# Kernel optimization log

Measured on AMD Instinct MI355X. Metric: run time of the kernel, lower is better.

Reference implementation:

```python
import jax, jax.numpy as jnp
import numpy as np

N = 100000   # neuron_count (nodes)
D = 128      # node feature dim
E = 2000000  # edges
NW = 8       # number of distinct weight matrices


def setup_inputs() -> dict:
    key = jax.random.key(0)
    k1, k2, k3, k4, k5 = jax.random.split(key, 5)
    x = jax.random.normal(k1, (N, D), dtype=jnp.float32)
    W = jax.random.normal(k2, (NW, D, D), dtype=jnp.float32) * 0.02
    u = jax.random.randint(k3, (E,), 0, N)      # edge source nodes
    v = jax.random.randint(k4, (E,), 0, N)      # edge dest nodes
    widx = jax.random.randint(k5, (E,), 0, NW)  # per-edge weight index
    return {"x": x, "W": W, "u": u, "v": v, "widx": widx}


def reference(x, W, u, v, widx):
    # DGL update_all: per-edge message m_e = W[widx_e] @ x[u_e], then
    # x_out[v] = tanh(sum of incoming m). Because the message is linear in
    # x_src, we aggregate source features per (weight-index, dest-node)
    # segment first, then apply each weight matrix once (grouped GEMM):
    #   out[v, i] = tanh( sum_w sum_j W[w, i, j] * S[w, v, j] )
    seg = widx * N + v                                   # combined segment id
    S = jax.ops.segment_sum(x[u], seg, num_segments=NW * N)  # [NW*N, D]
    S = S.reshape(NW, N, D)
    out = jnp.einsum("wij,wvj->vi", W, S)                # [N, D]
    # zero in-degree nodes: DGL gives 0 feature; tanh(0)=0, consistent.
    return jnp.tanh(out)
```

## Files before the change

### kernel.cpp

```cpp
#include <hip/hip_runtime.h>
#include <math.h>

#define D 128

typedef __attribute__((ext_vector_type(8))) short bf8;
typedef __attribute__((ext_vector_type(4))) float f32x4;

__device__ __forceinline__ unsigned short f2bf_rne(float f) {
  unsigned u = __float_as_uint(f);
  unsigned r = (u + 0x7FFFu + ((u >> 16) & 1u)) >> 16;
  return (unsigned short)r;
}
__device__ __forceinline__ float bf2f(unsigned short h) {
  return __uint_as_float(((unsigned)h) << 16);
}
__device__ __forceinline__ float bflo(unsigned p) {
  return __uint_as_float(p << 16);
}
__device__ __forceinline__ float bfhi(unsigned p) {
  return __uint_as_float(p & 0xFFFF0000u);
}

__global__ __launch_bounds__(256) void prep_kernel(
    const float* __restrict__ x, unsigned short* __restrict__ xbf,
    long long xTotal, int xcGrid,
    const int* __restrict__ v, const int* __restrict__ widx,
    int* __restrict__ cnt2, int* __restrict__ rank,
    long long E, long long N) {
  if (blockIdx.x < (unsigned)xcGrid) {
    long long i0 = ((long long)blockIdx.x * 256 + threadIdx.x) * 8;
    if (i0 + 8 > xTotal) return;
    float4 f0 = *(const float4*)(x + i0);
    float4 f1 = *(const float4*)(x + i0 + 4);
    unsigned short o[8];
    o[0] = f2bf_rne(f0.x); o[1] = f2bf_rne(f0.y);
    o[2] = f2bf_rne(f0.z); o[3] = f2bf_rne(f0.w);
    o[4] = f2bf_rne(f1.x); o[5] = f2bf_rne(f1.y);
    o[6] = f2bf_rne(f1.z); o[7] = f2bf_rne(f1.w);
    *(bf8*)(xbf + i0) = *(bf8*)o;
  } else {
    long long base = (long long)(blockIdx.x - xcGrid) * 1024;
    #pragma unroll
    for (int k = 0; k < 4; ++k) {
      long long e = base + k * 256 + threadIdx.x;
      if (e < E) {
        long long seg = (long long)widx[e] * N + v[e];
        rank[e] = atomicAdd(&cnt2[seg], 1);
      }
    }
  }
}

__global__ __launch_bounds__(1024) void scanA_kernel(
    const int* __restrict__ cnt2, int* __restrict__ starts2,
    int* __restrict__ blkSums, long long NB2) {
  __shared__ int part[1024];
  int tid = threadIdx.x;
  long long base = (long long)blockIdx.x * 4096 + tid * 4;
  int c[4];
  #pragma unroll
  for (int i = 0; i < 4; ++i)
    c[i] = (base + i < NB2) ? cnt2[base + i] : 0;
  int loc[4];
  int sum = 0;
  #pragma unroll
  for (int i = 0; i < 4; ++i) { loc[i] = sum; sum += c[i]; }
  part[tid] = sum;
  __syncthreads();
  for (int off = 1; off < 1024; off <<= 1) {
    int val = (tid >= off) ? part[tid - off] : 0;
    __syncthreads();
    part[tid] += val;
    __syncthreads();
  }
  int excl = (tid == 0) ? 0 : part[tid - 1];
  #pragma unroll
  for (int i = 0; i < 4; ++i)
    if (base + i < NB2) starts2[base + i] = excl + loc[i];
  if (tid == 1023) blkSums[blockIdx.x] = part[1023];
}

__global__ __launch_bounds__(1024) void scanC_kernel(
    int* __restrict__ starts2, const int* __restrict__ blkSums,
    long long NB2, int Etot, int nBlk) {
  __shared__ int part[256];
  int tid = threadIdx.x;
  if (tid < 256) part[tid] = (tid < nBlk) ? blkSums[tid] : 0;
  __syncthreads();
  for (int off = 1; off < 256; off <<= 1) {
    int val = 0;
    if (tid < 256 && tid >= off) val = part[tid - off];
    __syncthreads();
    if (tid < 256) part[tid] += val;
    __syncthreads();
  }
  int off = (blockIdx.x == 0) ? 0 : part[blockIdx.x - 1];
  long long base = (long long)blockIdx.x * 4096 + tid * 4;
  #pragma unroll
  for (int i = 0; i < 4; ++i) {
    long long idx = base + i;
    if (idx < NB2) starts2[idx] += off;
  }
  if (blockIdx.x == 0 && tid == 0) starts2[NB2] = Etot;
}

__global__ __launch_bounds__(256) void scatwc_kernel(
    const float* __restrict__ W, unsigned short* __restrict__ Wp, int NW,
    int wpGrid,
    const int* __restrict__ u, const int* __restrict__ v,
    const int* __restrict__ widx, const int* __restrict__ rank,
    const int* __restrict__ starts2, int* __restrict__ sortedU,
    long long E, long long N) {
  if (blockIdx.x < (unsigned)wpGrid) {
    int idx = blockIdx.x * 256 + threadIdx.x;
    if (idx >= NW * 2048) return;
    int lane = idx & 63;
    int ks = (idx >> 6) & 3;
    int n  = (idx >> 8) & 7;
    int w  = idx >> 11;
    int row = n * 16 + (lane & 15);
    int col = ks * 32 + (lane >> 4) * 8;
    const float* src = W + (size_t)w * D * D + (size_t)row * D + col;
    unsigned short hi[8], re[8];
    #pragma unroll
    for (int e = 0; e < 8; ++e) {
      float f = src[e];
      unsigned short h = f2bf_rne(f);
      hi[e] = h;
      re[e] = f2bf_rne(f - bf2f(h));
    }
    int frag = (w * 8 + n) * 4 + ks;
    unsigned short* dst = Wp + (size_t)frag * 1024 + lane * 8;
    *(bf8*)dst = *(bf8*)hi;
    *(bf8*)(dst + 512) = *(bf8*)re;
  } else {
    long long base = (long long)(blockIdx.x - wpGrid) * 1024;
    #pragma unroll
    for (int k = 0; k < 4; ++k) {
      long long e = base + k * 256 + threadIdx.x;
      if (e < E) {
        long long seg = (long long)widx[e] * N + v[e];
        int pos = starts2[seg] + rank[e];
        sortedU[pos] = u[e] * 32;
      }
    }
  }
}

__global__ __launch_bounds__(256) void gather_pack_kernel(
    const unsigned short* __restrict__ xbf, const int* __restrict__ starts2,
    const int* __restrict__ sortedU, unsigned short* __restrict__ Sp,
    long long N, long long nt16) {
  __shared__ float T[16][132];
  int tid = threadIdx.x;
  long long w = blockIdx.y;
  long long rt = blockIdx.x;
  long long r0 = rt * 16;
  int grp = tid >> 5;
  int lane = tid & 31;

  #pragma unroll
  for (int rr = 0; rr < 2; ++rr) {
    int rloc = grp + rr * 8;
    long long r = r0 + rloc;
    float ax = 0.f, ay = 0.f, az = 0.f, aw = 0.f;
    if (r < N) {
      long long seg = w * N + r;
      int s0 = starts2[seg];
      int s1 = starts2[seg + 1];
      const uint2* xb = (const uint2*)xbf;
      for (int i = s0; i < s1; i += 4) {
        int uu[4];
        uint2 av[4];
        #pragma unroll
        for (int k = 0; k < 4; ++k)
          if (i + k < s1) uu[k] = sortedU[i + k];
        #pragma unroll
        for (int k = 0; k < 4; ++k)
          if (i + k < s1) av[k] = xb[(size_t)uu[k] + lane];
        #pragma unroll
        for (int k = 0; k < 4; ++k) {
          if (i + k < s1) {
            ax += bflo(av[k].x); ay += bfhi(av[k].x);
            az += bflo(av[k].y); aw += bfhi(av[k].y);
          }
        }
      }
    }
    *(float4*)&T[rloc][lane * 4] = make_float4(ax, ay, az, aw);
  }
  __syncthreads();

  int ks = tid >> 6;
  int l = tid & 63;
  const float* src = &T[l & 15][ks * 32 + (l >> 4) * 8];
  unsigned short o[8];
  #pragma unroll
  for (int e = 0; e < 8; ++e) o[e] = f2bf_rne(src[e]);
  size_t frag = ((size_t)w * nt16 + rt) * 4 + ks;
  *(bf8*)(Sp + frag * 512 + (size_t)l * 8) = *(bf8*)o;
}

template<int NWT>
__global__ __launch_bounds__(256, 3) void mfma_gemm_kernel(
    const unsigned short* __restrict__ Sp, const unsigned short* __restrict__ Wp,
    float* __restrict__ out, long long N, long long nt16, int NWdyn) {
  int tid = threadIdx.x;
  int wv = tid >> 6;
  int wr = wv >> 1;
  int wc = wv & 1;
  int l = tid & 63;
  long long rtBase = (long long)blockIdx.x * 4 + wr * 2;

  const unsigned short* SA = Sp + (size_t)rtBase * 2048 + (size_t)l * 8;
  const unsigned short* WB = Wp + (size_t)wc * 16384 + (size_t)l * 8;
  const size_t wStrideS = (size_t)nt16 * 2048;

  f32x4 acc[2][4];
  #pragma unroll
  for (int m = 0; m < 2; ++m)
    #pragma unroll
    for (int n = 0; n < 4; ++n) acc[m][n] = (f32x4)(0.f);

  if (NWT == 8) {
    bf8 a[4][2], bh[2][4], br[2][4];
    {
      a[0][0] = *(const bf8*)(SA);
      a[0][1] = *(const bf8*)(SA + 2048);
      a[1][0] = *(const bf8*)(SA + 512);
      a[1][1] = *(const bf8*)(SA + 512 + 2048);
      a[2][0] = *(const bf8*)(SA + 1024);
      a[2][1] = *(const bf8*)(SA + 1024 + 2048);
      #pragma unroll
      for (int n = 0; n < 4; ++n) {
        bh[0][n] = *(const bf8*)(WB + n * 4096);
        br[0][n] = *(const bf8*)(WB + n * 4096 + 512);
      }
    }
    #pragma unroll
    for (int s = 0; s < 32; ++s) {
      const int abuf = s & 3;
      const int bbuf = s & 1;
      if (s + 3 < 32) {
        const int t = s + 3, w2 = t >> 2, ks2 = t & 3;
        const unsigned short* sa = SA + (size_t)w2 * wStrideS + ks2 * 512;
        a[(s + 3) & 3][0] = *(const bf8*)(sa);
        a[(s + 3) & 3][1] = *(const bf8*)(sa + 2048);
      }
      if (s + 1 < 32) {
        const int t = s + 1, w2 = t >> 2, ks2 = t & 3;
        const unsigned short* wb = WB + (size_t)w2 * 32768 + ks2 * 1024;
        #pragma unroll
        for (int n = 0; n < 4; ++n) {
          bh[bbuf ^ 1][n] = *(const bf8*)(wb + n * 4096);
          br[bbuf ^ 1][n] = *(const bf8*)(wb + n * 4096 + 512);
        }
      }
      #pragma unroll
      for (int n = 0; n < 4; ++n)
        #pragma unroll
        for (int m = 0; m < 2; ++m) {
          acc[m][n] = __builtin_amdgcn_mfma_f32_16x16x32_bf16(a[abuf][m], bh[bbuf][n], acc[m][n], 0, 0, 0);
          acc[m][n] = __builtin_amdgcn_mfma_f32_16x16x32_bf16(a[abuf][m], br[bbuf][n], acc[m][n], 0, 0, 0);
        }
    }
  } else {
    for (int w = 0; w < NWdyn; ++w) {
      #pragma unroll
      for (int ks = 0; ks < 4; ++ks) {
        const unsigned short* sa = SA + (size_t)w * wStrideS + ks * 512;
        bf8 a0 = *(const bf8*)(sa);
        bf8 a1 = *(const bf8*)(sa + 2048);
        const unsigned short* wb = WB + (size_t)w * 32768 + ks * 1024;
        #pragma unroll
        for (int n = 0; n < 4; ++n) {
          bf8 bh0 = *(const bf8*)(wb + n * 4096);
          bf8 br0 = *(const bf8*)(wb + n * 4096 + 512);
          acc[0][n] = __builtin_amdgcn_mfma_f32_16x16x32_bf16(a0, bh0, acc[0][n], 0, 0, 0);
          acc[1][n] = __builtin_amdgcn_mfma_f32_16x16x32_bf16(a1, bh0, acc[1][n], 0, 0, 0);
          acc[0][n] = __builtin_amdgcn_mfma_f32_16x16x32_bf16(a0, br0, acc[0][n], 0, 0, 0);
          acc[1][n] = __builtin_amdgcn_mfma_f32_16x16x32_bf16(a1, br0, acc[1][n], 0, 0, 0);
        }
      }
    }
  }

  int lrow = l & 15;
  int crow0 = (l >> 4) * 4;
  #pragma unroll
  for (int m = 0; m < 2; ++m) {
    long long vbase = (rtBase + m) * 16 + crow0;
    #pragma unroll
    for (int rr = 0; rr < 4; ++rr) {
      long long v = vbase + rr;
      if (v < N) {
        float* op = out + v * D + wc * 64 + lrow;
        #pragma unroll
        for (int n = 0; n < 4; ++n) op[n * 16] = tanhf(acc[m][n][rr]);
      }
    }
  }
}

extern "C" void kernel_launch(void* const* d_in, const int* in_sizes, int n_in,
                              void* d_out, int out_size, void* d_ws, size_t ws_size,
                              hipStream_t stream) {
  const float* x    = (const float*)d_in[0];
  const float* W    = (const float*)d_in[1];
  const int*   u    = (const int*)d_in[2];
  const int*   v    = (const int*)d_in[3];
  const int*   widx = (const int*)d_in[4];

  long long N  = (long long)in_sizes[0] / D;
  int       NW = in_sizes[1] / (D * D);
  long long E  = (long long)in_sizes[2];
  float* out = (float*)d_out;

  long long NB2 = (long long)NW * N;
  int gemmBlocks = (int)((N + 63) / 64);
  long long NpadA = (long long)gemmBlocks * 64;
  long long nt16 = NpadA / 16;
  int nScanBlk = (int)((NB2 + 4095) / 4096);
  long long xTotal = N * D;

  char* ws = (char*)d_ws;
  int* cnt2    = (int*)ws;                        ws += (size_t)NB2 * sizeof(int);
  int* starts2 = (int*)ws;                        ws += ((size_t)NB2 + 1) * sizeof(int);
  int* rank    = (int*)ws;                        ws += (size_t)E * sizeof(int);
  int* blkSums = (int*)ws;                        ws += 256 * sizeof(int);
  int* sortedU = (int*)ws;                        ws += (size_t)E * sizeof(int);
  ws = (char*)(((uintptr_t)ws + 255) & ~(uintptr_t)255);
  unsigned short* Wp = (unsigned short*)ws;       ws += (size_t)NW * 32768 * 2;
  ws = (char*)(((uintptr_t)ws + 255) & ~(uintptr_t)255);
  unsigned short* xbf = (unsigned short*)ws;      ws += (size_t)xTotal * 2;
  ws = (char*)(((uintptr_t)ws + 255) & ~(uintptr_t)255);
  unsigned short* Sp = (unsigned short*)ws;       ws += (size_t)NW * NpadA * D * 2;
  (void)ws_size;

  dim3 blk(256);
  int edgeGrid4 = (int)((E + 1023) / 1024);
  int wpGrid = (NW * 2048 + 255) / 256;
  int xcGrid = (int)((xTotal / 8 + 255) / 256);

  hipMemsetAsync(cnt2, 0, (size_t)NB2 * sizeof(int), stream);
  prep_kernel<<<xcGrid + edgeGrid4, blk, 0, stream>>>(
      x, xbf, xTotal, xcGrid, v, widx, cnt2, rank, E, N);
  scanA_kernel<<<nScanBlk, 1024, 0, stream>>>(cnt2, starts2, blkSums, NB2);
  scanC_kernel<<<nScanBlk, 1024, 0, stream>>>(starts2, blkSums, NB2,
                                              (int)E, nScanBlk);
  scatwc_kernel<<<wpGrid + edgeGrid4, blk, 0, stream>>>(
      W, Wp, NW, wpGrid, u, v, widx, rank, starts2, sortedU, E, N);
  dim3 ggrid((unsigned)nt16, (unsigned)NW);
  gather_pack_kernel<<<ggrid, blk, 0, stream>>>(xbf, starts2, sortedU, Sp, N, nt16);
  if (NW == 8) {
    mfma_gemm_kernel<8><<<gemmBlocks, blk, 0, stream>>>(
        Sp, Wp, out, N, nt16, NW);
  } else {
    mfma_gemm_kernel<0><<<gemmBlocks, blk, 0, stream>>>(
        Sp, Wp, out, N, nt16, NW);
  }
}
```

Before: 397.4 us.

## Stage GEMM A-tiles into LDS via async global_load_lds double buffering

The grouped GEMM kernel now copies each weight slice's S tile straight into shared memory with global_load_lds, double-buffered across the eight weight indices with a block barrier per stage, instead of having every wave load its A fragments into registers. This is meant to cut register pressure and overlap the A-tile fetch with MFMA work, and the occupancy hint rises from 3 to 4 blocks per CU. The cost is 32 KB of LDS per block and a __syncthreads every weight step. The per-lane A register prefetch is replaced by LDS reads.

```diff
diff --git a/kernel.cpp b/kernel.cpp
--- a/kernel.cpp
+++ b/kernel.cpp
@@ -5,6 +5,8 @@
 
 typedef __attribute__((ext_vector_type(8))) short bf8;
 typedef __attribute__((ext_vector_type(4))) float f32x4;
+typedef const __attribute__((address_space(1))) unsigned short* gas_us;
+typedef __attribute__((address_space(3))) unsigned short* las_us;
 
 __device__ __forceinline__ unsigned short f2bf_rne(float f) {
   unsigned u = __float_as_uint(f);
@@ -202,17 +204,17 @@
 }
 
 template<int NWT>
-__global__ __launch_bounds__(256, 3) void mfma_gemm_kernel(
+__global__ __launch_bounds__(256, 4) void mfma_gemm_kernel(
     const unsigned short* __restrict__ Sp, const unsigned short* __restrict__ Wp,
     float* __restrict__ out, long long N, long long nt16, int NWdyn) {
+  __shared__ unsigned short Al[2][8192];
   int tid = threadIdx.x;
   int wv = tid >> 6;
   int wr = wv >> 1;
   int wc = wv & 1;
   int l = tid & 63;
-  long long rtBase = (long long)blockIdx.x * 4 + wr * 2;
-
-  const unsigned short* SA = Sp + (size_t)rtBase * 2048 + (size_t)l * 8;
+  long long rtBlk = (long long)blockIdx.x * 4;
+
   const unsigned short* WB = Wp + (size_t)wc * 16384 + (size_t)l * 8;
   const size_t wStrideS = (size_t)nt16 * 2048;
 
@@ -223,48 +225,62 @@
     for (int n = 0; n < 4; ++n) acc[m][n] = (f32x4)(0.f);
 
   if (NWT == 8) {
-    bf8 a[4][2], bh[2][4], br[2][4];
-    {
-      a[0][0] = *(const bf8*)(SA);
-      a[0][1] = *(const bf8*)(SA + 2048);
-      a[1][0] = *(const bf8*)(SA + 512);
-      a[1][1] = *(const bf8*)(SA + 512 + 2048);
-      a[2][0] = *(const bf8*)(SA + 1024);
-      a[2][1] = *(const bf8*)(SA + 1024 + 2048);
+    #define STAGE_A(W_, B_)                                                  \
+      {                                                                      \
+        const unsigned short* g =                                            \
+            Sp + ((size_t)(W_) * nt16 + rtBlk) * 2048;                       \
+        _Pragma("unroll")                                                    \
+        for (int c = 0; c < 4; ++c) {                                        \
+          int chunk = wv * 4 + c;                                            \
+          __builtin_amdgcn_global_load_lds(                                  \
+              (gas_us)(g + chunk * 512 + l * 8),                             \
+              (las_us)&Al[B_][chunk * 512], 16, 0, 0);                       \
+        }                                                                    \
+      }
+
+    STAGE_A(0, 0)
+    __syncthreads();
+
+    bf8 bh[2][4], br[2][4];
+    #pragma unroll
+    for (int n = 0; n < 4; ++n) {
+      bh[0][n] = *(const bf8*)(WB + n * 4096);
+      br[0][n] = *(const bf8*)(WB + n * 4096 + 512);
+    }
+
+    #pragma unroll
+    for (int w = 0; w < 8; ++w) {
+      if (w < 7) STAGE_A(w + 1, (w + 1) & 1)
+      const int b = w & 1;
+      int rtl = wr * 2;
       #pragma unroll
-      for (int n = 0; n < 4; ++n) {
-        bh[0][n] = *(const bf8*)(WB + n * 4096);
-        br[0][n] = *(const bf8*)(WB + n * 4096 + 512);
-      }
-    }
-    #pragma unroll
-    for (int s = 0; s < 32; ++s) {
-      const int abuf = s & 3;
-      const int bbuf = s & 1;
-      if (s + 3 < 32) {
-        const int t = s + 3, w2 = t >> 2, ks2 = t & 3;
-        const unsigned short* sa = SA + (size_t)w2 * wStrideS + ks2 * 512;
-        a[(s + 3) & 3][0] = *(const bf8*)(sa);
-        a[(s + 3) & 3][1] = *(const bf8*)(sa + 2048);
-      }
-      if (s + 1 < 32) {
-        const int t = s + 1, w2 = t >> 2, ks2 = t & 3;
-        const unsigned short* wb = WB + (size_t)w2 * 32768 + ks2 * 1024;
+      for (int ks = 0; ks < 4; ++ks) {
+        const int s = w * 4 + ks;
+        const int bb = s & 1;
+        if (s + 1 < 32) {
+          const int t = s + 1, w2 = t >> 2, ks2 = t & 3;
+          const unsigned short* wb = WB + (size_t)w2 * 32768 + ks2 * 1024;
+          #pragma unroll
+          for (int n = 0; n < 4; ++n) {
+            bh[bb ^ 1][n] = *(const bf8*)(wb + n * 4096);
+            br[bb ^ 1][n] = *(const bf8*)(wb + n * 4096 + 512);
+          }
+        }
+        bf8 a0 = *(const bf8*)&Al[b][(rtl * 4 + ks) * 512 + l * 8];
+        bf8 a1 = *(const bf8*)&Al[b][((rtl + 1) * 4 + ks) * 512 + l * 8];
         #pragma unroll
         for (int n = 0; n < 4; ++n) {
-          bh[bbuf ^ 1][n] = *(const bf8*)(wb + n * 4096);
-          br[bbuf ^ 1][n] = *(const bf8*)(wb + n * 4096 + 512);
+          acc[0][n] = __builtin_amdgcn_mfma_f32_16x16x32_bf16(a0, bh[bb][n], acc[0][n], 0, 0, 0);
+          acc[1][n] = __builtin_amdgcn_mfma_f32_16x16x32_bf16(a1, bh[bb][n], acc[1][n], 0, 0, 0);
+          acc[0][n] = __builtin_amdgcn_mfma_f32_16x16x32_bf16(a0, br[bb][n], acc[0][n], 0, 0, 0);
+          acc[1][n] = __builtin_amdgcn_mfma_f32_16x16x32_bf16(a1, br[bb][n], acc[1][n], 0, 0, 0);
         }
       }
-      #pragma unroll
-      for (int n = 0; n < 4; ++n)
-        #pragma unroll
-        for (int m = 0; m < 2; ++m) {
-          acc[m][n] = __builtin_amdgcn_mfma_f32_16x16x32_bf16(a[abuf][m], bh[bbuf][n], acc[m][n], 0, 0, 0);
-          acc[m][n] = __builtin_amdgcn_mfma_f32_16x16x32_bf16(a[abuf][m], br[bbuf][n], acc[m][n], 0, 0, 0);
-        }
-    }
+      __syncthreads();
+    }
+    #undef STAGE_A
   } else {
+    const unsigned short* SA = Sp + (size_t)(rtBlk + wr * 2) * 2048 + (size_t)l * 8;
     for (int w = 0; w < NWdyn; ++w) {
       #pragma unroll
       for (int ks = 0; ks < 4; ++ks) {
@@ -289,7 +305,7 @@
   int crow0 = (l >> 4) * 4;
   #pragma unroll
   for (int m = 0; m < 2; ++m) {
-    long long vbase = (rtBase + m) * 16 + crow0;
+    long long vbase = (rtBlk + wr * 2 + m) * 16 + crow0;
     #pragma unroll
     for (int rr = 0; rr < 4; ++rr) {
       long long v = vbase + rr;
```

Result: faster. 375.4 us (-5.6%).
